# Kernel optimization log

Hardware: AMD Instinct MI355X
Metric: run time of the kernel (lower is better)

Reference implementation:

```python
import jax, jax.numpy as jnp
import numpy as np

B, N, DIM = 2, 2048, 2048
H, KVH, HD = 16, 4, 128
N_REP = H // KVH
SCALE = np.float32(HD ** -0.5)


def setup_inputs() -> dict:
    key = jax.random.key(0)
    ks = jax.random.split(key, 5)
    x = jax.random.normal(ks[0], (B, N, DIM), dtype=jnp.float32)
    mask = jnp.tril(jnp.ones((N, N), dtype=jnp.int32))[None, None]  # [1,1,N,N] causal
    Wq = jax.random.normal(ks[1], (DIM, H * HD), dtype=jnp.float32) * (DIM ** -0.5)
    Wk = jax.random.normal(ks[2], (DIM, KVH * HD), dtype=jnp.float32) * (DIM ** -0.5)
    Wv = jax.random.normal(ks[3], (DIM, KVH * HD), dtype=jnp.float32) * (DIM ** -0.5)
    Wo = jax.random.normal(ks[4], (H * HD, DIM), dtype=jnp.float32) * ((H * HD) ** -0.5)
    return {"x": x, "mask": mask, "Wq": Wq, "Wk": Wk, "Wv": Wv, "Wo": Wo}


def reference(x, mask, Wq, Wk, Wv, Wo):
    Bx, Nx, _ = x.shape
    # projections -> [B, heads, N, head_dim]
    q = (x @ Wq).reshape(Bx, Nx, H, HD).transpose(0, 2, 1, 3)
    k = (x @ Wk).reshape(Bx, Nx, KVH, HD).transpose(0, 2, 1, 3)
    v = (x @ Wv).reshape(Bx, Nx, KVH, HD).transpose(0, 2, 1, 3)
    # repeat_interleave KV heads to match query heads (GQA)
    k = jnp.repeat(k, N_REP, axis=1)
    v = jnp.repeat(v, N_REP, axis=1)
    attn = jnp.einsum('bhqd,bhkd->bhqk', q, k) * SCALE
    attn = jnp.where(mask == 0, jnp.float32(-jnp.inf), attn)
    attn = jax.nn.softmax(attn, axis=-1)
    out = jnp.einsum('bhqk,bhkd->bhqd', attn, v)
    out = out.transpose(0, 2, 1, 3).reshape(Bx, Nx, H * HD)
    return out @ Wo
```

## Files before the change

### kernel.cpp

```cpp
#include <hip/hip_runtime.h>
#include <hip/hip_bf16.h>
#include <math.h>

typedef __bf16 bf16;
typedef bf16 bf16x8 __attribute__((ext_vector_type(8)));
typedef bf16 bf16x4v __attribute__((ext_vector_type(4)));
typedef float f32x4 __attribute__((ext_vector_type(4)));

#define GLD16(g, l) __builtin_amdgcn_global_load_lds(                          \
    (__attribute__((address_space(1))) void*)(g),                              \
    (__attribute__((address_space(3))) void*)(l), 16, 0, 0)

#define MFMA16(a, b, c) __builtin_amdgcn_mfma_f32_16x16x32_bf16((a), (b), (c), 0, 0, 0)

#if __has_builtin(__builtin_amdgcn_exp2f)
#define EXP2F(x) __builtin_amdgcn_exp2f(x)
#else
#define EXP2F(x) exp2f(x)
#endif

__device__ __forceinline__ f32x4 shfl_xor4(f32x4 a, int m) {
  f32x4 r;
  #pragma unroll
  for (int i = 0; i < 4; i++) r[i] = __shfl_xor(a[i], m);
  return r;
}

__global__ void cast_f32_bf16(const float* __restrict__ in, bf16* __restrict__ out, int n4) {
  int i = blockIdx.x * blockDim.x + threadIdx.x;
  if (i < n4) {
    float4 v = ((const float4*)in)[i];
    bf16x4v o;
    o.x = (bf16)v.x; o.y = (bf16)v.y; o.z = (bf16)v.z; o.w = (bf16)v.w;
    ((bf16x4v*)out)[i] = o;
  }
}

__global__ void transpose_cast(const float* __restrict__ in, bf16* __restrict__ out,
                               int colsIn, int outStride, int outRowOff, float scale) {
  __shared__ float t[32][33];
  int c0 = blockIdx.x * 32, r0 = blockIdx.y * 32;
  int tx = threadIdx.x, ty = threadIdx.y;
  #pragma unroll
  for (int i = 0; i < 32; i += 8)
    t[ty + i][tx] = in[(size_t)(r0 + ty + i) * colsIn + (c0 + tx)];
  __syncthreads();
  #pragma unroll
  for (int i = 0; i < 32; i += 8)
    out[(size_t)(outRowOff + c0 + ty + i) * outStride + (r0 + tx)] = (bf16)(t[tx][ty + i] * scale);
}

__global__ void transpose_v(const bf16* __restrict__ QKV, bf16* __restrict__ Vg) {
  __shared__ bf16 t[32][34];
  int n0 = blockIdx.x * 32, d0 = blockIdx.y * 32;
  int bk = blockIdx.z;
  int b = bk >> 2, kvh = bk & 3;
  const bf16* src = QKV + (size_t)b * 2048 * 3072 + 2560 + kvh * 128;
  bf16* dst = Vg + (size_t)bk * 128 * 2048;
  int tx = threadIdx.x, ty = threadIdx.y;
  #pragma unroll
  for (int i = 0; i < 32; i += 8)
    t[ty + i][tx] = src[(size_t)(n0 + ty + i) * 3072 + (d0 + tx)];
  __syncthreads();
  #pragma unroll
  for (int i = 0; i < 32; i += 8)
    dst[(size_t)(d0 + ty + i) * 2048 + (n0 + tx)] = t[tx][ty + i];
}

template <typename OutT>
__global__ __launch_bounds__(256, 2) void gemm_bt(const bf16* __restrict__ A,
                                                  const bf16* __restrict__ Bt,
                                                  OutT* __restrict__ C,
                                                  int M, int N, int K) {
  __shared__ __attribute__((aligned(16))) bf16 As[128 * 32];
  __shared__ __attribute__((aligned(16))) bf16 Bs[128 * 32];
  const int tid = threadIdx.x;
  const int lane = tid & 63;
  const int wave = tid >> 6;
  const int wm = wave >> 1, wn = wave & 1;
  const int l15 = lane & 15, quad = lane >> 4;
  const int rowBase = blockIdx.y * 128;
  const int colBase = blockIdx.x * 128;

  f32x4 acc[4][4] = {};

  const int cb0 = wave * 64;
  const int c0 = cb0 + lane;
  const int c1 = c0 + 256;
  const bf16* a0 = A + (size_t)(rowBase + (c0 >> 2)) * K + (c0 & 3) * 8;
  const bf16* a1 = A + (size_t)(rowBase + (c1 >> 2)) * K + (c1 & 3) * 8;
  const bf16* b0 = Bt + (size_t)(colBase + (c0 >> 2)) * K + (c0 & 3) * 8;
  const bf16* b1 = Bt + (size_t)(colBase + (c1 >> 2)) * K + (c1 & 3) * 8;
  bf16* lA0 = &As[cb0 * 8];
  bf16* lA1 = &As[(cb0 + 256) * 8];
  bf16* lB0 = &Bs[cb0 * 8];
  bf16* lB1 = &Bs[(cb0 + 256) * 8];

  for (int k0 = 0; k0 < K; k0 += 32) {
    GLD16(a0 + k0, lA0);
    GLD16(a1 + k0, lA1);
    GLD16(b0 + k0, lB0);
    GLD16(b1 + k0, lB1);
    __syncthreads();
    bf16x8 af[4], bfr[4];
    #pragma unroll
    for (int i = 0; i < 4; i++)
      af[i] = *(const bf16x8*)&As[(wm * 64 + i * 16 + l15) * 32 + quad * 8];
    #pragma unroll
    for (int i = 0; i < 4; i++)
      bfr[i] = *(const bf16x8*)&Bs[(wn * 64 + i * 16 + l15) * 32 + quad * 8];
    #pragma unroll
    for (int i = 0; i < 4; i++)
      #pragma unroll
      for (int j = 0; j < 4; j++)
        acc[i][j] = MFMA16(af[i], bfr[j], acc[i][j]);
    __syncthreads();
  }

  #pragma unroll
  for (int i = 0; i < 4; i++) {
    int row = rowBase + wm * 64 + i * 16 + quad * 4;
    #pragma unroll
    for (int j = 0; j < 4; j++) {
      int col = colBase + wn * 64 + j * 16 + l15;
      #pragma unroll
      for (int r = 0; r < 4; r++)
        C[(size_t)(row + r) * N + col] = (OutT)acc[i][j][r];
    }
  }
}

#define MASKV (-1e30f)

__global__ __launch_bounds__(256, 2) void gqa_attn(const bf16* __restrict__ QKV,
                                                   const bf16* __restrict__ Vg,
                                                   bf16* __restrict__ Obf) {
  __shared__ __attribute__((aligned(16))) bf16 Kl[64 * 128];
  __shared__ __attribute__((aligned(16))) bf16 Vt[128 * 64];
  __shared__ __attribute__((aligned(16))) bf16 Pl[4][32 * 68];

  const int tid = threadIdx.x;
  const int lane = tid & 63;
  const int wave = tid >> 6;
  const int l15 = lane & 15, quad = lane >> 4;

  int bi = blockIdx.x;
  int bh = bi & 31;
  int jj = (bi & 255) >> 5;
  int qt = (bi < 256) ? (8 + jj) : (7 - jj);
  int b = bh >> 4, h = bh & 15, kvh = h >> 2;
  int q0 = qt * 128;

  const size_t rs = 3072;
  const bf16* Qb  = QKV + (size_t)b * 2048 * rs + h * 128;
  const bf16* Kb  = QKV + (size_t)b * 2048 * rs + 2048 + kvh * 128;
  const bf16* Vgb = Vg + (size_t)(b * 4 + kvh) * 128 * 2048;

  bf16x8 qf[2][4];
  #pragma unroll
  for (int mt = 0; mt < 2; mt++) {
    int row = q0 + wave * 32 + mt * 16 + l15;
    #pragma unroll
    for (int ks = 0; ks < 4; ks++)
      qf[mt][ks] = *(const bf16x8*)&Qb[(size_t)row * rs + ks * 32 + quad * 8];
  }

  const bf16* kp[4]; const bf16* vp[4];
  bf16* kl[4]; bf16* vl[4];
  #pragma unroll
  for (int t = 0; t < 4; t++) {
    int keyl = wave * 16 + t * 4 + (lane >> 4);
    int ck = (lane & 15) ^ (4 * (t & 1) + (lane >> 4));
    kp[t] = Kb + (size_t)keyl * rs + ck * 8;
    kl[t] = &Kl[(wave * 16 + t * 4) * 128];
    int dl = wave * 32 + t * 8 + (lane >> 3);
    int cv = (lane & 7) ^ (lane >> 3);
    vp[t] = Vgb + (size_t)dl * 2048 + cv * 8;
    vl[t] = &Vt[(wave * 32 + t * 8) * 64];
  }

  f32x4 oacc[2][8] = {};
  f32x4 mrow[2], lrow[2];
  #pragma unroll
  for (int mt = 0; mt < 2; mt++)
    #pragma unroll
    for (int r = 0; r < 4; r++) { mrow[mt][r] = MASKV; lrow[mt][r] = 0.f; }

  const int nkt = 2 * qt + 2;
  const int myrow_hi = q0 + wave * 32 + 31;
  for (int kt = 0; kt < nkt; kt++) {
    const int k0 = kt * 64;
    __syncthreads();
    #pragma unroll
    for (int t = 0; t < 4; t++) { GLD16(kp[t], kl[t]); kp[t] += 64 * rs; }
    #pragma unroll
    for (int t = 0; t < 4; t++) { GLD16(vp[t], vl[t]); vp[t] += 64; }
    __syncthreads();

    if (k0 > myrow_hi) continue;

    f32x4 s[2][4] = {};
    #pragma unroll
    for (int ks = 0; ks < 4; ks++) {
      #pragma unroll
      for (int nt = 0; nt < 4; nt++) {
        bf16x8 kf = *(const bf16x8*)&Kl[(nt * 16 + l15) * 128 +
                                        (((ks * 4 + quad) ^ (l15 & 7)) * 8)];
        s[0][nt] = MFMA16(qf[0][ks], kf, s[0][nt]);
        s[1][nt] = MFMA16(qf[1][ks], kf, s[1][nt]);
      }
    }
    if (kt >= nkt - 2) {
      #pragma unroll
      for (int mt = 0; mt < 2; mt++) {
        int rowb = q0 + wave * 32 + mt * 16 + quad * 4;
        #pragma unroll
        for (int nt = 0; nt < 4; nt++) {
          int col = k0 + nt * 16 + l15;
          #pragma unroll
          for (int r = 0; r < 4; r++)
            if (col > rowb + r) s[mt][nt][r] = MASKV;
        }
      }
    }
    #pragma unroll
    for (int mt = 0; mt < 2; mt++) {
      f32x4 mx = s[mt][0];
      #pragma unroll
      for (int nt = 1; nt < 4; nt++)
        #pragma unroll
        for (int r = 0; r < 4; r++) mx[r] = fmaxf(mx[r], s[mt][nt][r]);
      #pragma unroll
      for (int d = 1; d < 16; d <<= 1) {
        f32x4 o = shfl_xor4(mx, d);
        #pragma unroll
        for (int r = 0; r < 4; r++) mx[r] = fmaxf(mx[r], o[r]);
      }
      f32x4 mnew, alpha;
      #pragma unroll
      for (int r = 0; r < 4; r++) {
        mnew[r] = fmaxf(mrow[mt][r], mx[r]);
        alpha[r] = EXP2F(mrow[mt][r] - mnew[r]);
      }
      f32x4 rsum = {0.f, 0.f, 0.f, 0.f};
      #pragma unroll
      for (int nt = 0; nt < 4; nt++)
        #pragma unroll
        for (int r = 0; r < 4; r++) {
          float p = EXP2F(s[mt][nt][r] - mnew[r]);
          s[mt][nt][r] = p;
          rsum[r] += p;
        }
      #pragma unroll
      for (int d = 1; d < 16; d <<= 1) rsum += shfl_xor4(rsum, d);
      #pragma unroll
      for (int r = 0; r < 4; r++) {
        lrow[mt][r] = lrow[mt][r] * alpha[r] + rsum[r];
        mrow[mt][r] = mnew[r];
      }
      #pragma unroll
      for (int no = 0; no < 8; no++)
        #pragma unroll
        for (int r = 0; r < 4; r++) oacc[mt][no][r] *= alpha[r];
      #pragma unroll
      for (int nt = 0; nt < 4; nt++)
        #pragma unroll
        for (int r = 0; r < 4; r++)
          Pl[wave][(mt * 16 + quad * 4 + r) * 68 + nt * 16 + l15] = (bf16)s[mt][nt][r];
    }
    #pragma unroll
    for (int ks2 = 0; ks2 < 2; ks2++) {
      bf16x8 pf0 = *(const bf16x8*)&Pl[wave][l15 * 68 + ks2 * 32 + quad * 8];
      bf16x8 pf1 = *(const bf16x8*)&Pl[wave][(16 + l15) * 68 + ks2 * 32 + quad * 8];
      #pragma unroll
      for (int no = 0; no < 8; no++) {
        bf16x8 vf = *(const bf16x8*)&Vt[(no * 16 + l15) * 64 +
                                        (((ks2 * 4 + quad) ^ (l15 & 7)) * 8)];
        oacc[0][no] = MFMA16(pf0, vf, oacc[0][no]);
        oacc[1][no] = MFMA16(pf1, vf, oacc[1][no]);
      }
    }
  }

  #pragma unroll
  for (int mt = 0; mt < 2; mt++) {
    f32x4 linv;
    #pragma unroll
    for (int r = 0; r < 4; r++) linv[r] = 1.0f / lrow[mt][r];
    int row = q0 + wave * 32 + mt * 16 + quad * 4;
    #pragma unroll
    for (int no = 0; no < 8; no++) {
      int col = h * 128 + no * 16 + l15;
      #pragma unroll
      for (int r = 0; r < 4; r++)
        Obf[(size_t)(b * 2048 + row + r) * 2048 + col] = (bf16)(oacc[mt][no][r] * linv[r]);
    }
  }
}

extern "C" void kernel_launch(void* const* d_in, const int* in_sizes, int n_in,
                              void* d_out, int out_size, void* d_ws, size_t ws_size,
                              hipStream_t stream) {
  const float* x  = (const float*)d_in[0];
  const float* Wq = (const float*)d_in[2];
  const float* Wk = (const float*)d_in[3];
  const float* Wv = (const float*)d_in[4];
  const float* Wo = (const float*)d_in[5];
  float* out = (float*)d_out;

  bf16* Xb    = (bf16*)d_ws;
  bf16* Wqkvt = Xb + 8388608;
  bf16* Wot   = Wqkvt + 6291456;
  bf16* QKV   = Wot + 4194304;
  bf16* Obf   = QKV + 12582912;
  bf16* Vg    = Obf + 8388608;

  const float qscale = (float)(0.08838834764831845 * 1.4426950408889634);

  cast_f32_bf16<<<8192, 256, 0, stream>>>(x, Xb, 2097152);
  dim3 tb(32, 8);
  transpose_cast<<<dim3(64, 64), tb, 0, stream>>>(Wq, Wqkvt, 2048, 2048, 0, qscale);
  transpose_cast<<<dim3(16, 64), tb, 0, stream>>>(Wk, Wqkvt, 512, 2048, 2048, 1.0f);
  transpose_cast<<<dim3(16, 64), tb, 0, stream>>>(Wv, Wqkvt, 512, 2048, 2560, 1.0f);
  transpose_cast<<<dim3(64, 64), tb, 0, stream>>>(Wo, Wot, 2048, 2048, 0, 1.0f);

  gemm_bt<bf16><<<dim3(24, 32), 256, 0, stream>>>(Xb, Wqkvt, QKV, 4096, 3072, 2048);
  transpose_v<<<dim3(64, 4, 8), tb, 0, stream>>>(QKV, Vg);
  gqa_attn<<<512, 256, 0, stream>>>(QKV, Vg, Obf);
  gemm_bt<float><<<dim3(16, 32), 256, 0, stream>>>(Obf, Wot, out, 4096, 2048, 2048);
}
```

Before: 339.0 us.

## Compute transposed scores so P stays in registers, use fp16 PV MFMA

Swaps the MFMA operands for QK^T so each lane holds one query row's scores. The softmax probabilities can then feed the PV MFMA directly from registers as f16x4 operands, which removes the per-wave LDS staging buffer for P. V is converted to fp16 in the transpose step, and the V LDS layout uses a rotation swizzle. Row max and sum reductions drop to two shuffles of scalars, launch bounds rise to 3 blocks per SM, the block-to-tile order becomes a simple heaviest-first schedule, and output stores are vectorized. The risks are fp16 precision for P and V, and the silent no-op fallback if the f16 MFMA builtin is missing.

```diff
diff --git a/kernel.cpp b/kernel.cpp
--- a/kernel.cpp
+++ b/kernel.cpp
@@ -6,6 +6,8 @@
 typedef bf16 bf16x8 __attribute__((ext_vector_type(8)));
 typedef bf16 bf16x4v __attribute__((ext_vector_type(4)));
 typedef float f32x4 __attribute__((ext_vector_type(4)));
+typedef _Float16 f16;
+typedef f16 f16x4 __attribute__((ext_vector_type(4)));
 
 #define GLD16(g, l) __builtin_amdgcn_global_load_lds(                          \
     (__attribute__((address_space(1))) void*)(g),                              \
@@ -13,18 +15,13 @@
 
 #define MFMA16(a, b, c) __builtin_amdgcn_mfma_f32_16x16x32_bf16((a), (b), (c), 0, 0, 0)
 
-#if __has_builtin(__builtin_amdgcn_exp2f)
-#define EXP2F(x) __builtin_amdgcn_exp2f(x)
+#if __has_builtin(__builtin_amdgcn_mfma_f32_16x16x16_f16)
+#define MFMA16F16(a, b, c) __builtin_amdgcn_mfma_f32_16x16x16_f16((a), (b), (c), 0, 0, 0)
+#elif __has_builtin(__builtin_amdgcn_mfma_f32_16x16x16f16)
+#define MFMA16F16(a, b, c) __builtin_amdgcn_mfma_f32_16x16x16f16((a), (b), (c), 0, 0, 0)
 #else
-#define EXP2F(x) exp2f(x)
+__host__ __device__ static inline f32x4 MFMA16F16(f16x4 a, f16x4 b, f32x4 c) { return c; }
 #endif
-
-__device__ __forceinline__ f32x4 shfl_xor4(f32x4 a, int m) {
-  f32x4 r;
-  #pragma unroll
-  for (int i = 0; i < 4; i++) r[i] = __shfl_xor(a[i], m);
-  return r;
-}
 
 __global__ void cast_f32_bf16(const float* __restrict__ in, bf16* __restrict__ out, int n4) {
   int i = blockIdx.x * blockDim.x + threadIdx.x;
@@ -50,13 +47,13 @@
     out[(size_t)(outRowOff + c0 + ty + i) * outStride + (r0 + tx)] = (bf16)(t[tx][ty + i] * scale);
 }
 
-__global__ void transpose_v(const bf16* __restrict__ QKV, bf16* __restrict__ Vg) {
+__global__ void transpose_v(const bf16* __restrict__ QKV, f16* __restrict__ Vg) {
   __shared__ bf16 t[32][34];
   int n0 = blockIdx.x * 32, d0 = blockIdx.y * 32;
   int bk = blockIdx.z;
   int b = bk >> 2, kvh = bk & 3;
   const bf16* src = QKV + (size_t)b * 2048 * 3072 + 2560 + kvh * 128;
-  bf16* dst = Vg + (size_t)bk * 128 * 2048;
+  f16* dst = Vg + (size_t)bk * 128 * 2048;
   int tx = threadIdx.x, ty = threadIdx.y;
   #pragma unroll
   for (int i = 0; i < 32; i += 8)
@@ -64,7 +61,7 @@
   __syncthreads();
   #pragma unroll
   for (int i = 0; i < 32; i += 8)
-    dst[(size_t)(d0 + ty + i) * 2048 + (n0 + tx)] = t[tx][ty + i];
+    dst[(size_t)(d0 + ty + i) * 2048 + (n0 + tx)] = (f16)(float)t[tx][ty + i];
 }
 
 template <typename OutT>
@@ -132,12 +129,11 @@
 
 #define MASKV (-1e30f)
 
-__global__ __launch_bounds__(256, 2) void gqa_attn(const bf16* __restrict__ QKV,
-                                                   const bf16* __restrict__ Vg,
+__global__ __launch_bounds__(256, 3) void gqa_attn(const bf16* __restrict__ QKV,
+                                                   const f16* __restrict__ Vg,
                                                    bf16* __restrict__ Obf) {
   __shared__ __attribute__((aligned(16))) bf16 Kl[64 * 128];
-  __shared__ __attribute__((aligned(16))) bf16 Vt[128 * 64];
-  __shared__ __attribute__((aligned(16))) bf16 Pl[4][32 * 68];
+  __shared__ __attribute__((aligned(16))) f16  Vt[128 * 64];
 
   const int tid = threadIdx.x;
   const int lane = tid & 63;
@@ -145,16 +141,15 @@
   const int l15 = lane & 15, quad = lane >> 4;
 
   int bi = blockIdx.x;
+  int qt = 15 - (bi >> 5);
   int bh = bi & 31;
-  int jj = (bi & 255) >> 5;
-  int qt = (bi < 256) ? (8 + jj) : (7 - jj);
   int b = bh >> 4, h = bh & 15, kvh = h >> 2;
   int q0 = qt * 128;
 
   const size_t rs = 3072;
   const bf16* Qb  = QKV + (size_t)b * 2048 * rs + h * 128;
   const bf16* Kb  = QKV + (size_t)b * 2048 * rs + 2048 + kvh * 128;
-  const bf16* Vgb = Vg + (size_t)(b * 4 + kvh) * 128 * 2048;
+  const f16*  Vgb = Vg + (size_t)(b * 4 + kvh) * 128 * 2048;
 
   bf16x8 qf[2][4];
   #pragma unroll
@@ -165,8 +160,8 @@
       qf[mt][ks] = *(const bf16x8*)&Qb[(size_t)row * rs + ks * 32 + quad * 8];
   }
 
-  const bf16* kp[4]; const bf16* vp[4];
-  bf16* kl[4]; bf16* vl[4];
+  const bf16* kp[4]; const f16* vp[4];
+  bf16* kl[4]; f16* vl[4];
   #pragma unroll
   for (int t = 0; t < 4; t++) {
     int keyl = wave * 16 + t * 4 + (lane >> 4);
@@ -174,17 +169,13 @@
     kp[t] = Kb + (size_t)keyl * rs + ck * 8;
     kl[t] = &Kl[(wave * 16 + t * 4) * 128];
     int dl = wave * 32 + t * 8 + (lane >> 3);
-    int cv = (lane & 7) ^ (lane >> 3);
-    vp[t] = Vgb + (size_t)dl * 2048 + cv * 8;
+    int g = ((lane & 7) - (dl & 7)) & 7;
+    vp[t] = Vgb + (size_t)dl * 2048 + g * 8;
     vl[t] = &Vt[(wave * 32 + t * 8) * 64];
   }
 
   f32x4 oacc[2][8] = {};
-  f32x4 mrow[2], lrow[2];
-  #pragma unroll
-  for (int mt = 0; mt < 2; mt++)
-    #pragma unroll
-    for (int r = 0; r < 4; r++) { mrow[mt][r] = MASKV; lrow[mt][r] = 0.f; }
+  float mst[2] = {MASKV, MASKV}, lst[2] = {0.f, 0.f};
 
   const int nkt = 2 * qt + 2;
   const int myrow_hi = q0 + wave * 32 + 31;
@@ -206,94 +197,83 @@
       for (int nt = 0; nt < 4; nt++) {
         bf16x8 kf = *(const bf16x8*)&Kl[(nt * 16 + l15) * 128 +
                                         (((ks * 4 + quad) ^ (l15 & 7)) * 8)];
-        s[0][nt] = MFMA16(qf[0][ks], kf, s[0][nt]);
-        s[1][nt] = MFMA16(qf[1][ks], kf, s[1][nt]);
+        s[0][nt] = MFMA16(kf, qf[0][ks], s[0][nt]);
+        s[1][nt] = MFMA16(kf, qf[1][ks], s[1][nt]);
       }
     }
     if (kt >= nkt - 2) {
       #pragma unroll
       for (int mt = 0; mt < 2; mt++) {
-        int rowb = q0 + wave * 32 + mt * 16 + quad * 4;
+        int qrow = q0 + wave * 32 + mt * 16 + l15;
         #pragma unroll
         for (int nt = 0; nt < 4; nt++) {
-          int col = k0 + nt * 16 + l15;
+          int keyb = k0 + nt * 16 + quad * 4;
           #pragma unroll
           for (int r = 0; r < 4; r++)
-            if (col > rowb + r) s[mt][nt][r] = MASKV;
+            if (keyb + r > qrow) s[mt][nt][r] = MASKV;
         }
       }
     }
+    f16x4 pa[2][4];
     #pragma unroll
     for (int mt = 0; mt < 2; mt++) {
-      f32x4 mx = s[mt][0];
-      #pragma unroll
-      for (int nt = 1; nt < 4; nt++)
-        #pragma unroll
-        for (int r = 0; r < 4; r++) mx[r] = fmaxf(mx[r], s[mt][nt][r]);
-      #pragma unroll
-      for (int d = 1; d < 16; d <<= 1) {
-        f32x4 o = shfl_xor4(mx, d);
-        #pragma unroll
-        for (int r = 0; r < 4; r++) mx[r] = fmaxf(mx[r], o[r]);
+      float mloc = MASKV;
+      #pragma unroll
+      for (int nt = 0; nt < 4; nt++)
+        #pragma unroll
+        for (int r = 0; r < 4; r++) mloc = fmaxf(mloc, s[mt][nt][r]);
+      mloc = fmaxf(mloc, __shfl_xor(mloc, 16));
+      mloc = fmaxf(mloc, __shfl_xor(mloc, 32));
+      float mnew = fmaxf(mst[mt], mloc);
+      float alpha = exp2f(mst[mt] - mnew);
+      float rsum = 0.f;
+      #pragma unroll
+      for (int nt = 0; nt < 4; nt++)
+        #pragma unroll
+        for (int r = 0; r < 4; r++) {
+          float p = exp2f(s[mt][nt][r] - mnew);
+          s[mt][nt][r] = p;
+          rsum += p;
+        }
+      rsum += __shfl_xor(rsum, 16);
+      rsum += __shfl_xor(rsum, 32);
+      lst[mt] = lst[mt] * alpha + rsum;
+      mst[mt] = mnew;
+      #pragma unroll
+      for (int no = 0; no < 8; no++)
+        #pragma unroll
+        for (int r = 0; r < 4; r++) oacc[mt][no][r] *= alpha;
+      #pragma unroll
+      for (int nt = 0; nt < 4; nt++) {
+        f16x4 p4;
+        #pragma unroll
+        for (int r = 0; r < 4; r++) p4[r] = (f16)s[mt][nt][r];
+        pa[mt][nt] = p4;
       }
-      f32x4 mnew, alpha;
-      #pragma unroll
-      for (int r = 0; r < 4; r++) {
-        mnew[r] = fmaxf(mrow[mt][r], mx[r]);
-        alpha[r] = EXP2F(mrow[mt][r] - mnew[r]);
+    }
+    #pragma unroll
+    for (int nt = 0; nt < 4; nt++) {
+      #pragma unroll
+      for (int no = 0; no < 8; no++) {
+        f16x4 vf = *(const f16x4*)&Vt[(no * 16 + l15) * 64 +
+                                      (((nt * 4 + quad) + 2 * (l15 & 7)) & 15) * 4];
+        oacc[0][no] = MFMA16F16(vf, pa[0][nt], oacc[0][no]);
+        oacc[1][no] = MFMA16F16(vf, pa[1][nt], oacc[1][no]);
       }
-      f32x4 rsum = {0.f, 0.f, 0.f, 0.f};
-      #pragma unroll
-      for (int nt = 0; nt < 4; nt++)
-        #pragma unroll
-        for (int r = 0; r < 4; r++) {
-          float p = EXP2F(s[mt][nt][r] - mnew[r]);
-          s[mt][nt][r] = p;
-          rsum[r] += p;
-        }
-      #pragma unroll
-      for (int d = 1; d < 16; d <<= 1) rsum += shfl_xor4(rsum, d);
-      #pragma unroll
-      for (int r = 0; r < 4; r++) {
-        lrow[mt][r] = lrow[mt][r] * alpha[r] + rsum[r];
-        mrow[mt][r] = mnew[r];
-      }
-      #pragma unroll
-      for (int no = 0; no < 8; no++)
-        #pragma unroll
-        for (int r = 0; r < 4; r++) oacc[mt][no][r] *= alpha[r];
-      #pragma unroll
-      for (int nt = 0; nt < 4; nt++)
-        #pragma unroll
-        for (int r = 0; r < 4; r++)
-          Pl[wave][(mt * 16 + quad * 4 + r) * 68 + nt * 16 + l15] = (bf16)s[mt][nt][r];
-    }
-    #pragma unroll
-    for (int ks2 = 0; ks2 < 2; ks2++) {
-      bf16x8 pf0 = *(const bf16x8*)&Pl[wave][l15 * 68 + ks2 * 32 + quad * 8];
-      bf16x8 pf1 = *(const bf16x8*)&Pl[wave][(16 + l15) * 68 + ks2 * 32 + quad * 8];
-      #pragma unroll
-      for (int no = 0; no < 8; no++) {
-        bf16x8 vf = *(const bf16x8*)&Vt[(no * 16 + l15) * 64 +
-                                        (((ks2 * 4 + quad) ^ (l15 & 7)) * 8)];
-        oacc[0][no] = MFMA16(pf0, vf, oacc[0][no]);
-        oacc[1][no] = MFMA16(pf1, vf, oacc[1][no]);
-      }
     }
   }
 
   #pragma unroll
   for (int mt = 0; mt < 2; mt++) {
-    f32x4 linv;
-    #pragma unroll
-    for (int r = 0; r < 4; r++) linv[r] = 1.0f / lrow[mt][r];
-    int row = q0 + wave * 32 + mt * 16 + quad * 4;
+    float linv = 1.0f / lst[mt];
+    int qrow = q0 + wave * 32 + mt * 16 + l15;
+    bf16* orow = Obf + (size_t)(b * 2048 + qrow) * 2048 + h * 128 + quad * 4;
     #pragma unroll
     for (int no = 0; no < 8; no++) {
-      int col = h * 128 + no * 16 + l15;
-      #pragma unroll
-      for (int r = 0; r < 4; r++)
-        Obf[(size_t)(b * 2048 + row + r) * 2048 + col] = (bf16)(oacc[mt][no][r] * linv[r]);
+      bf16x4v o4;
+      #pragma unroll
+      for (int r = 0; r < 4; r++) o4[r] = (bf16)(oacc[mt][no][r] * linv);
+      *(bf16x4v*)(orow + no * 16) = o4;
     }
   }
 }
@@ -313,7 +293,7 @@
   bf16* Wot   = Wqkvt + 6291456;
   bf16* QKV   = Wot + 4194304;
   bf16* Obf   = QKV + 12582912;
-  bf16* Vg    = Obf + 8388608;
+  f16*  Vg    = (f16*)(Obf + 8388608);
 
   const float qscale = (float)(0.08838834764831845 * 1.4426950408889634);
 
```

Measured after the change: 390.1 us. 1.15x slower.
